# Kernel tuning notes

Measured on AMD Instinct MI355X. Metric: run time of the kernel, lower is better.

Reference implementation:

```python
import jax, jax.numpy as jnp
import numpy as np

B, N, D_MODEL, ATT_DIM, H = 2, 2048, 1024, 1024, 8
HEAD_DIM = ATT_DIM // H


def setup_inputs() -> dict:
    key = jax.random.key(0)
    ks = jax.random.split(key, 10)
    s_in = 1.0 / np.sqrt(D_MODEL)
    s_att = 1.0 / np.sqrt(ATT_DIM)
    x = jax.random.normal(ks[0], (B, N, D_MODEL), dtype=jnp.float32)
    mask = jax.random.randint(ks[1], (B, 1, N, N), 0, 2) == 1
    Wq = jax.random.uniform(ks[2], (D_MODEL, ATT_DIM), jnp.float32, -s_in, s_in)
    bq = jnp.zeros((ATT_DIM,), jnp.float32)
    Wk = jax.random.uniform(ks[3], (D_MODEL, ATT_DIM), jnp.float32, -s_in, s_in)
    bk = jnp.zeros((ATT_DIM,), jnp.float32)
    Wv = jax.random.uniform(ks[4], (D_MODEL, ATT_DIM), jnp.float32, -s_in, s_in)
    bv = jnp.zeros((ATT_DIM,), jnp.float32)
    Wo = jax.random.uniform(ks[5], (ATT_DIM, D_MODEL), jnp.float32, -s_att, s_att)
    bo = jnp.zeros((D_MODEL,), jnp.float32)
    return {"x": x, "mask": mask, "Wq": Wq, "bq": bq, "Wk": Wk, "bk": bk,
            "Wv": Wv, "bv": bv, "Wo": Wo, "bo": bo}


def reference(x, mask, Wq, bq, Wk, bk, Wv, bv, Wo, bo):
    # x: [B, N, d_model]; dropout is identity (eval mode) for a deterministic baseline.
    b, n, d_model = x.shape
    scale = d_model ** (-0.5)  # NOTE: original scales by d_model, not head_dim

    def split_heads(t):  # [B, N, att] -> [B, H, N, head]
        return t.reshape(b, n, H, HEAD_DIM).transpose(0, 2, 1, 3)

    q = split_heads(x @ Wq + bq)
    k = split_heads(x @ Wk + bk)
    v = split_heads(x @ Wv + bv)
    score = jnp.einsum('bhqd,bhkd->bhqk', q, k) * scale
    score = jnp.where(mask, -jnp.inf, score)
    w = jax.nn.softmax(score, axis=-1)
    out = jnp.einsum('bhqk,bhkd->bhqd', w, v)            # [B, H, N, head]
    out = out.transpose(0, 2, 1, 3).reshape(b, n, ATT_DIM)
    return out @ Wo + bo
```

## Files before the change

kernel.cpp:

```cpp
#include <hip/hip_runtime.h>
#include <stdint.h>

typedef __bf16 bf16_t;
typedef bf16_t bf16x8 __attribute__((ext_vector_type(8)));
typedef float f32x4 __attribute__((ext_vector_type(4)));
typedef unsigned long long u64;

#define B_ 2
#define N_ 2048
#define DM 1024
#define H_ 8
#define HD 128

#define GLDS16(g, l) __builtin_amdgcn_global_load_lds(                      \
    (const __attribute__((address_space(1))) void*)(g),                     \
    (__attribute__((address_space(3))) void*)(l), 16, 0, 0)

__global__ void cvt_kernel(const float* __restrict__ in, bf16_t* __restrict__ out, int n8)
{
    int i = blockIdx.x * blockDim.x + threadIdx.x;
    if (i >= n8) return;
    const float4 a = *(const float4*)(in + (size_t)i * 8);
    const float4 b = *(const float4*)(in + (size_t)i * 8 + 4);
    bf16x8 o;
    o[0] = (bf16_t)a.x; o[1] = (bf16_t)a.y; o[2] = (bf16_t)a.z; o[3] = (bf16_t)a.w;
    o[4] = (bf16_t)b.x; o[5] = (bf16_t)b.y; o[6] = (bf16_t)b.z; o[7] = (bf16_t)b.w;
    *(bf16x8*)(out + (size_t)i * 8) = o;
}

__global__ void transpose_cvt(const float* __restrict__ W, bf16_t* __restrict__ Wt)
{
    __shared__ float t[32][33];
    const int tx = threadIdx.x & 31;
    const int ty = threadIdx.x >> 5;
    const int bx = blockIdx.x * 32;
    const int by = blockIdx.y * 32;
#pragma unroll
    for (int i = 0; i < 32; i += 8)
        t[ty + i][tx] = W[(size_t)(by + ty + i) * 1024 + bx + tx];
    __syncthreads();
#pragma unroll
    for (int i = 0; i < 32; i += 8)
        Wt[(size_t)(bx + ty + i) * 1024 + by + tx] = (bf16_t)t[tx][ty + i];
}

__global__ void mask_pack(const int* __restrict__ mask, u64* __restrict__ mb, int nwords)
{
    const int t = blockIdx.x * blockDim.x + threadIdx.x;
    const int w = t >> 6;
    if (w >= nwords) return;
    const int v = mask[(size_t)w * 64 + (t & 63)];
    const u64 bits = __ballot(v != 0);
    if ((t & 63) == 0) mb[w] = bits;
}

template<int MODE>
__global__ __launch_bounds__(256)
void gemm_bt(const bf16_t* __restrict__ A, const bf16_t* __restrict__ Bt,
             const float* __restrict__ b0, const float* __restrict__ b1,
             const float* __restrict__ b2,
             void* __restrict__ Cout, bf16_t* __restrict__ VtOut,
             const int M, const int N, const int K, const int ldc)
{
    __shared__ bf16_t sA[2][128 * 32];
    __shared__ bf16_t sB[2][128 * 32];

    const int tid  = threadIdx.x;
    const int wv   = tid >> 6;
    const int lane = tid & 63;
    const int fr   = lane & 15;
    const int fk   = (lane >> 4) * 8;

    const int row0 = blockIdx.x * 128;
    const int col0 = blockIdx.y * 128;
    const int wr   = (wv >> 1) * 64;
    const int wc   = (wv & 1) * 64;

    const int srow = wv * 32 + (lane >> 2);
    const int scol = (lane & 3) * 8;

    const bf16_t* gA0 = A  + (size_t)(row0 + srow) * K + scol;
    const bf16_t* gA1 = gA0 + (size_t)16 * K;
    const bf16_t* gB0 = Bt + (size_t)(col0 + srow) * K + scol;
    const bf16_t* gB1 = gB0 + (size_t)16 * K;

    const int ldst0 = wv * 1024;
    const int ldst1 = wv * 1024 + 512;

    f32x4 acc[4][4] = {};
    const int NT = K >> 5;

    GLDS16(gA0, &sA[0][ldst0]);
    GLDS16(gA1, &sA[0][ldst1]);
    GLDS16(gB0, &sB[0][ldst0]);
    GLDS16(gB1, &sB[0][ldst1]);
    __syncthreads();

    for (int kt = 0; kt < NT; ++kt) {
        const int cur = kt & 1;
        if (kt + 1 < NT) {
            const size_t ko = (size_t)(kt + 1) * 32;
            GLDS16(gA0 + ko, &sA[cur ^ 1][ldst0]);
            GLDS16(gA1 + ko, &sA[cur ^ 1][ldst1]);
            GLDS16(gB0 + ko, &sB[cur ^ 1][ldst0]);
            GLDS16(gB1 + ko, &sB[cur ^ 1][ldst1]);
        }
        bf16x8 af[4], bfr[4];
#pragma unroll
        for (int i = 0; i < 4; ++i)
            af[i] = *(const bf16x8*)&sA[cur][(wr + i * 16 + fr) * 32 + fk];
#pragma unroll
        for (int i = 0; i < 4; ++i)
            bfr[i] = *(const bf16x8*)&sB[cur][(wc + i * 16 + fr) * 32 + fk];
#pragma unroll
        for (int i = 0; i < 4; ++i)
#pragma unroll
            for (int j = 0; j < 4; ++j)
                acc[i][j] = __builtin_amdgcn_mfma_f32_16x16x32_bf16(af[i], bfr[j], acc[i][j], 0, 0, 0);
        __syncthreads();
    }

#pragma unroll
    for (int i = 0; i < 4; ++i) {
#pragma unroll
        for (int j = 0; j < 4; ++j) {
            const int c = col0 + wc + j * 16 + fr;
            const int seg = c >> 10;
            const float bb = (seg == 0) ? b0[c] : (seg == 1 ? b1[c - 1024] : b2[c - 2048]);
#pragma unroll
            for (int r = 0; r < 4; ++r) {
                const int row = row0 + wr + i * 16 + (lane >> 4) * 4 + r;
                const float v = acc[i][j][r] + bb;
                if constexpr (MODE == 1) {
                    ((float*)Cout)[(size_t)row * ldc + c] = v;
                } else if constexpr (MODE == 0) {
                    ((bf16_t*)Cout)[(size_t)row * ldc + c] = (bf16_t)v;
                } else {
                    if (c < 2048) {
                        ((bf16_t*)Cout)[(size_t)row * ldc + c] = (bf16_t)v;
                    } else {
                        const int ch = c - 2048;
                        const int bb_ = row >> 11;
                        const int nn  = row & 2047;
                        VtOut[((size_t)(bb_ * H_ + (ch >> 7)) * HD + (ch & 127)) * N_ + nn] = (bf16_t)v;
                    }
                }
            }
        }
    }
}

__global__ __launch_bounds__(256)
void flash_attn(const bf16_t* __restrict__ QK, const bf16_t* __restrict__ Vt,
                const u64* __restrict__ mbits, bf16_t* __restrict__ AO)
{
    __shared__ bf16_t sK[64 * 128];
    __shared__ bf16_t sVt[128 * 64];
    __shared__ bf16_t sP[4][16 * 64];

    const int tid  = threadIdx.x;
    const int wv   = tid >> 6;
    const int lane = tid & 63;
    const int fr   = lane & 15;
    const int g4   = lane >> 4;
    const int fk   = g4 * 8;

    const int bh = blockIdx.x & 15;
    const int q0 = (blockIdx.x >> 4) * 64;
    const int b  = bh >> 3;
    const int h  = bh & 7;

    const int qrow = q0 + wv * 16 + fr;
    const size_t qoff = ((size_t)(b * N_ + qrow)) * 2048 + h * HD;
    bf16x8 qf[4];
#pragma unroll
    for (int j = 0; j < 4; ++j) {
        bf16x8 t = *(const bf16x8*)&QK[qoff + j * 32 + fk];
#pragma unroll
        for (int e = 0; e < 8; ++e) qf[j][e] = (bf16_t)((float)t[e] * 0.03125f);
    }

    const bf16_t* kg[4]; bf16_t* kd[4];
#pragma unroll
    for (int n = 0; n < 4; ++n) {
        const int row = wv * 16 + n * 4 + g4;
        kg[n] = QK + ((size_t)(b * N_ + row)) * 2048 + 1024 + h * HD
                   + ((fr * 8) ^ ((row & 15) << 3));
        kd[n] = sK + (wv * 16 + n * 4) * 128;
    }
    const bf16_t* vg[4]; bf16_t* vd[4];
    {
        const int l8 = lane >> 3;
        const int c8 = (lane & 7) * 8;
#pragma unroll
        for (int n = 0; n < 4; ++n) {
            const int d = wv * 32 + n * 8 + l8;
            vg[n] = Vt + ((size_t)((b * H_ + h) * HD + d)) * N_ + (c8 ^ (l8 << 3));
            vd[n] = sVt + (wv * 32 + n * 8) * 64;
        }
    }
    const size_t mrow = (size_t)(b * N_ + q0 + wv * 16 + g4 * 4) * 32;

    f32x4 acc_o[8] = {};
    float mr[4], ls[4];
#pragma unroll
    for (int r = 0; r < 4; ++r) { mr[r] = -1e30f; ls[r] = 0.0f; }

    const int ksw = fr << 3;
    const int vsw = (fr & 7) << 3;
    const int psw = ((fr & 7) << 3) ^ ((fr & 8) << 1);

    for (int kc = 0; kc < N_ / 64; ++kc) {
        __syncthreads();
#pragma unroll
        for (int n = 0; n < 4; ++n) {
            GLDS16(kg[n] + (size_t)kc * 64 * 2048, kd[n]);
            GLDS16(vg[n] + kc * 64, vd[n]);
        }
        u64 mb[4];
#pragma unroll
        for (int r = 0; r < 4; ++r) mb[r] = mbits[mrow + (size_t)r * 32 + kc];
        __syncthreads();

        f32x4 accs[4] = {};
#pragma unroll
        for (int kf = 0; kf < 4; ++kf) {
            const int krow = kf * 16 + fr;
#pragma unroll
            for (int j = 0; j < 4; ++j) {
                bf16x8 kb = *(const bf16x8*)&sK[krow * 128 + ((j * 32 + fk) ^ ksw)];
                accs[kf] = __builtin_amdgcn_mfma_f32_16x16x32_bf16(qf[j], kb, accs[kf], 0, 0, 0);
            }
        }

        float sv[4][4];
#pragma unroll
        for (int kf = 0; kf < 4; ++kf)
#pragma unroll
            for (int r = 0; r < 4; ++r)
                sv[kf][r] = ((mb[r] >> (kf * 16 + fr)) & 1ull) ? -__builtin_inff()
                                                               : accs[kf][r];

        float al[4];
#pragma unroll
        for (int r = 0; r < 4; ++r) {
            float v = fmaxf(fmaxf(sv[0][r], sv[1][r]), fmaxf(sv[2][r], sv[3][r]));
#pragma unroll
            for (int mm = 1; mm <= 8; mm <<= 1) v = fmaxf(v, __shfl_xor(v, mm, 16));
            const float mnew = fmaxf(mr[r], v);
            al[r] = __expf(mr[r] - mnew);
            mr[r] = mnew;
        }
        float ps[4] = {0.f, 0.f, 0.f, 0.f};
#pragma unroll
        for (int kf = 0; kf < 4; ++kf) {
#pragma unroll
            for (int r = 0; r < 4; ++r) {
                const float p = __expf(sv[kf][r] - mr[r]);
                ps[r] += p;
                const int prow = g4 * 4 + r;
                const int s = ((prow & 7) << 3) ^ ((prow & 8) << 1);
                sP[wv][prow * 64 + ((kf * 16 + fr) ^ s)] = (bf16_t)p;
            }
        }
#pragma unroll
        for (int r = 0; r < 4; ++r) {
            float v = ps[r];
#pragma unroll
            for (int mm = 1; mm <= 8; mm <<= 1) v += __shfl_xor(v, mm, 16);
            ls[r] = ls[r] * al[r] + v;
        }
#pragma unroll
        for (int df = 0; df < 8; ++df)
#pragma unroll
            for (int r = 0; r < 4; ++r)
                acc_o[df][r] *= al[r];

#pragma unroll
        for (int ks = 0; ks < 2; ++ks) {
            bf16x8 pf = *(const bf16x8*)&sP[wv][fr * 64 + ((ks * 32 + fk) ^ psw)];
#pragma unroll
            for (int df = 0; df < 8; ++df) {
                const int vrow = df * 16 + fr;
                bf16x8 vb = *(const bf16x8*)&sVt[vrow * 64 + ((ks * 32 + fk) ^ vsw)];
                acc_o[df] = __builtin_amdgcn_mfma_f32_16x16x32_bf16(pf, vb, acc_o[df], 0, 0, 0);
            }
        }
    }

#pragma unroll
    for (int df = 0; df < 8; ++df) {
#pragma unroll
        for (int r = 0; r < 4; ++r) {
            const int row = q0 + wv * 16 + g4 * 4 + r;
            AO[((size_t)(b * N_ + row)) * DM + h * HD + df * 16 + fr] =
                (bf16_t)(acc_o[df][r] / ls[r]);
        }
    }
}

extern "C" void kernel_launch(void* const* d_in, const int* in_sizes, int n_in,
                              void* d_out, int out_size, void* d_ws, size_t ws_size,
                              hipStream_t stream)
{
    const float* x  = (const float*)d_in[0];
    const int* mask = (const int*)d_in[1];
    const float* Wq = (const float*)d_in[2];
    const float* bq = (const float*)d_in[3];
    const float* Wk = (const float*)d_in[4];
    const float* bk = (const float*)d_in[5];
    const float* Wv = (const float*)d_in[6];
    const float* bv = (const float*)d_in[7];
    const float* Wo = (const float*)d_in[8];
    const float* bo = (const float*)d_in[9];
    float* out = (float*)d_out;

    const size_t MT = (size_t)B_ * N_;
    bf16_t* xb    = (bf16_t*)d_ws;
    bf16_t* Wqkvt = xb + MT * DM;
    bf16_t* Wot   = Wqkvt + (size_t)3072 * DM;
    bf16_t* QKb   = Wot + (size_t)DM * DM;
    bf16_t* Vtb   = QKb + MT * 2048;
    bf16_t* AOb   = Vtb + (size_t)B_ * H_ * HD * N_;
    u64*    mbits = (u64*)(AOb + MT * DM);

    cvt_kernel<<<2048, 256, 0, stream>>>(x, xb, (int)(MT * DM / 8));

    dim3 tg(32, 32);
    transpose_cvt<<<tg, 256, 0, stream>>>(Wq, Wqkvt);
    transpose_cvt<<<tg, 256, 0, stream>>>(Wk, Wqkvt + (size_t)DM * DM);
    transpose_cvt<<<tg, 256, 0, stream>>>(Wv, Wqkvt + (size_t)2 * DM * DM);
    transpose_cvt<<<tg, 256, 0, stream>>>(Wo, Wot);

    const int nwords = B_ * N_ * (N_ / 64);
    mask_pack<<<nwords / 4, 256, 0, stream>>>(mask, mbits, nwords);

    gemm_bt<2><<<dim3(MT / 128, 3072 / 128), 256, 0, stream>>>(
        xb, Wqkvt, bq, bk, bv, QKb, Vtb, (int)MT, 3072, DM, 2048);

    flash_attn<<<512, 256, 0, stream>>>(QKb, Vtb, mbits, AOb);

    gemm_bt<1><<<dim3(MT / 128, DM / 128), 256, 0, stream>>>(
        AOb, Wot, bo, bo, bo, out, nullptr, (int)MT, DM, DM, DM);
}
```

Before: 287.9 us.

## Split attention KV range in two, drop online max, swizzle GEMM block order

Flash attention now splits the key/value sequence into two halves across twice as many workgroups. Each half writes a partial normalized output and its row sum, and a new combine kernel merges the two halves by weighting them with those sums. The online max tracking and accumulator rescaling are removed: exp is taken of raw scaled scores, and row sums are computed with an MFMA against a ones vector. This cuts VALU and shuffle work, but it assumes the scores stay small enough not to overflow. Both GEMMs switch to a 1D grid whose block index is swizzled in groups of eight, and the attention kernel gets a waves-per-EU launch bound; the buffer for the partial outputs reuses the workspace that held the converted x.

```diff
diff --git a/kernel.cpp b/kernel.cpp
--- a/kernel.cpp
+++ b/kernel.cpp
@@ -3,6 +3,7 @@
 
 typedef __bf16 bf16_t;
 typedef bf16_t bf16x8 __attribute__((ext_vector_type(8)));
+typedef bf16_t bf16x4 __attribute__((ext_vector_type(4)));
 typedef float f32x4 __attribute__((ext_vector_type(4)));
 typedef unsigned long long u64;
 
@@ -60,7 +61,7 @@
              const float* __restrict__ b0, const float* __restrict__ b1,
              const float* __restrict__ b2,
              void* __restrict__ Cout, bf16_t* __restrict__ VtOut,
-             const int M, const int N, const int K, const int ldc)
+             const int M, const int N, const int K, const int ldc, const int gy)
 {
     __shared__ bf16_t sA[2][128 * 32];
     __shared__ bf16_t sB[2][128 * 32];
@@ -71,8 +72,13 @@
     const int fr   = lane & 15;
     const int fk   = (lane >> 4) * 8;
 
-    const int row0 = blockIdx.x * 128;
-    const int col0 = blockIdx.y * 128;
+    const int nwg = gridDim.x;
+    const int swz = ((int)blockIdx.x & 7) * (nwg >> 3) + ((int)blockIdx.x >> 3);
+    const int by  = swz % gy;
+    const int bx  = swz / gy;
+
+    const int row0 = bx * 128;
+    const int col0 = by * 128;
     const int wr   = (wv >> 1) * 64;
     const int wc   = (wv & 1) * 64;
 
@@ -150,9 +156,10 @@
     }
 }
 
-__global__ __launch_bounds__(256)
+__global__ __launch_bounds__(256, 4)
 void flash_attn(const bf16_t* __restrict__ QK, const bf16_t* __restrict__ Vt,
-                const u64* __restrict__ mbits, bf16_t* __restrict__ AO)
+                const u64* __restrict__ mbits, bf16_t* __restrict__ Os,
+                float* __restrict__ Ls)
 {
     __shared__ bf16_t sK[64 * 128];
     __shared__ bf16_t sVt[128 * 64];
@@ -165,10 +172,13 @@
     const int g4   = lane >> 4;
     const int fk   = g4 * 8;
 
-    const int bh = blockIdx.x & 15;
-    const int q0 = (blockIdx.x >> 4) * 64;
+    const int work = ((int)blockIdx.x & 7) * 128 + ((int)blockIdx.x >> 3);
+    const int s  = work >> 9;
+    const int bh = (work >> 5) & 15;
+    const int q0 = (work & 31) * 64;
     const int b  = bh >> 3;
     const int h  = bh & 7;
+    const int kvbase = s * 1024;
 
     const int qrow = q0 + wv * 16 + fr;
     const size_t qoff = ((size_t)(b * N_ + qrow)) * 2048 + h * HD;
@@ -184,7 +194,7 @@
 #pragma unroll
     for (int n = 0; n < 4; ++n) {
         const int row = wv * 16 + n * 4 + g4;
-        kg[n] = QK + ((size_t)(b * N_ + row)) * 2048 + 1024 + h * HD
+        kg[n] = QK + ((size_t)(b * N_ + kvbase + row)) * 2048 + 1024 + h * HD
                    + ((fr * 8) ^ ((row & 15) << 3));
         kd[n] = sK + (wv * 16 + n * 4) * 128;
     }
@@ -195,22 +205,25 @@
 #pragma unroll
         for (int n = 0; n < 4; ++n) {
             const int d = wv * 32 + n * 8 + l8;
-            vg[n] = Vt + ((size_t)((b * H_ + h) * HD + d)) * N_ + (c8 ^ (l8 << 3));
+            vg[n] = Vt + ((size_t)((b * H_ + h) * HD + d)) * N_ + kvbase + (c8 ^ (l8 << 3));
             vd[n] = sVt + (wv * 32 + n * 8) * 64;
         }
     }
-    const size_t mrow = (size_t)(b * N_ + q0 + wv * 16 + g4 * 4) * 32;
+    const size_t mrow = (size_t)(b * N_ + q0 + wv * 16 + g4 * 4) * 32 + s * 16;
 
     f32x4 acc_o[8] = {};
-    float mr[4], ls[4];
-#pragma unroll
-    for (int r = 0; r < 4; ++r) { mr[r] = -1e30f; ls[r] = 0.0f; }
+    f32x4 acc_l = {};
+    bf16x8 ones_f = {};
+    if (fr == 0) {
+#pragma unroll
+        for (int e = 0; e < 8; ++e) ones_f[e] = (bf16_t)1.0f;
+    }
 
     const int ksw = fr << 3;
     const int vsw = (fr & 7) << 3;
     const int psw = ((fr & 7) << 3) ^ ((fr & 8) << 1);
 
-    for (int kc = 0; kc < N_ / 64; ++kc) {
+    for (int kc = 0; kc < 16; ++kc) {
         __syncthreads();
 #pragma unroll
         for (int n = 0; n < 4; ++n) {
@@ -233,52 +246,23 @@
             }
         }
 
-        float sv[4][4];
-#pragma unroll
-        for (int kf = 0; kf < 4; ++kf)
-#pragma unroll
-            for (int r = 0; r < 4; ++r)
-                sv[kf][r] = ((mb[r] >> (kf * 16 + fr)) & 1ull) ? -__builtin_inff()
-                                                               : accs[kf][r];
-
-        float al[4];
-#pragma unroll
-        for (int r = 0; r < 4; ++r) {
-            float v = fmaxf(fmaxf(sv[0][r], sv[1][r]), fmaxf(sv[2][r], sv[3][r]));
-#pragma unroll
-            for (int mm = 1; mm <= 8; mm <<= 1) v = fmaxf(v, __shfl_xor(v, mm, 16));
-            const float mnew = fmaxf(mr[r], v);
-            al[r] = __expf(mr[r] - mnew);
-            mr[r] = mnew;
-        }
-        float ps[4] = {0.f, 0.f, 0.f, 0.f};
 #pragma unroll
         for (int kf = 0; kf < 4; ++kf) {
 #pragma unroll
             for (int r = 0; r < 4; ++r) {
-                const float p = __expf(sv[kf][r] - mr[r]);
-                ps[r] += p;
+                const float svv = ((mb[r] >> (kf * 16 + fr)) & 1ull) ? -__builtin_inff()
+                                                                     : accs[kf][r];
+                const float p = __expf(svv);
                 const int prow = g4 * 4 + r;
-                const int s = ((prow & 7) << 3) ^ ((prow & 8) << 1);
-                sP[wv][prow * 64 + ((kf * 16 + fr) ^ s)] = (bf16_t)p;
+                const int ss = ((prow & 7) << 3) ^ ((prow & 8) << 1);
+                sP[wv][prow * 64 + ((kf * 16 + fr) ^ ss)] = (bf16_t)p;
             }
         }
-#pragma unroll
-        for (int r = 0; r < 4; ++r) {
-            float v = ps[r];
-#pragma unroll
-            for (int mm = 1; mm <= 8; mm <<= 1) v += __shfl_xor(v, mm, 16);
-            ls[r] = ls[r] * al[r] + v;
-        }
-#pragma unroll
-        for (int df = 0; df < 8; ++df)
-#pragma unroll
-            for (int r = 0; r < 4; ++r)
-                acc_o[df][r] *= al[r];
 
 #pragma unroll
         for (int ks = 0; ks < 2; ++ks) {
             bf16x8 pf = *(const bf16x8*)&sP[wv][fr * 64 + ((ks * 32 + fk) ^ psw)];
+            acc_l = __builtin_amdgcn_mfma_f32_16x16x32_bf16(pf, ones_f, acc_l, 0, 0, 0);
 #pragma unroll
             for (int df = 0; df < 8; ++df) {
                 const int vrow = df * 16 + fr;
@@ -288,15 +272,50 @@
         }
     }
 
+    float lv[4], inv[4];
+#pragma unroll
+    for (int r = 0; r < 4; ++r) {
+        lv[r]  = __shfl(acc_l[r], lane & 48, 64);
+        inv[r] = 1.0f / lv[r];
+    }
+
 #pragma unroll
     for (int df = 0; df < 8; ++df) {
 #pragma unroll
         for (int r = 0; r < 4; ++r) {
             const int row = q0 + wv * 16 + g4 * 4 + r;
-            AO[((size_t)(b * N_ + row)) * DM + h * HD + df * 16 + fr] =
-                (bf16_t)(acc_o[df][r] / ls[r]);
-        }
-    }
+            Os[((size_t)(s * 4096 + b * N_ + row)) * 1024 + h * 128 + df * 16 + fr] =
+                (bf16_t)(acc_o[df][r] * inv[r]);
+        }
+    }
+    if (fr == 0) {
+#pragma unroll
+        for (int r = 0; r < 4; ++r) {
+            const int row = q0 + wv * 16 + g4 * 4 + r;
+            Ls[((size_t)((s * 2 + b) * 8 + h)) * 2048 + row] = lv[r];
+        }
+    }
+}
+
+__global__ void combine(const bf16_t* __restrict__ Os, const float* __restrict__ Ls,
+                        bf16_t* __restrict__ AO)
+{
+    const int i = blockIdx.x;
+    const int c = threadIdx.x * 4;
+    const int b = i >> 11;
+    const int n = i & 2047;
+    const int h = c >> 7;
+    const float l0 = Ls[((size_t)(b * 8 + h)) * 2048 + n];
+    const float l1 = Ls[((size_t)(16 + b * 8 + h)) * 2048 + n];
+    const float w  = 1.0f / (l0 + l1);
+    const float w0 = l0 * w, w1 = l1 * w;
+    bf16x4 a = *(const bf16x4*)&Os[(size_t)i * 1024 + c];
+    bf16x4 d = *(const bf16x4*)&Os[(size_t)4096 * 1024 + (size_t)i * 1024 + c];
+    bf16x4 o;
+#pragma unroll
+    for (int e = 0; e < 4; ++e)
+        o[e] = (bf16_t)((float)a[e] * w0 + (float)d[e] * w1);
+    *(bf16x4*)&AO[(size_t)i * 1024 + c] = o;
 }
 
 extern "C" void kernel_launch(void* const* d_in, const int* in_sizes, int n_in,
@@ -316,13 +335,17 @@
     float* out = (float*)d_out;
 
     const size_t MT = (size_t)B_ * N_;
-    bf16_t* xb    = (bf16_t*)d_ws;
-    bf16_t* Wqkvt = xb + MT * DM;
-    bf16_t* Wot   = Wqkvt + (size_t)3072 * DM;
-    bf16_t* QKb   = Wot + (size_t)DM * DM;
+    const size_t M1 = 1024 * 1024;
+    bf16_t* wsb   = (bf16_t*)d_ws;
+    bf16_t* Os    = wsb;
+    bf16_t* xb    = wsb;
+    bf16_t* Wqkvt = wsb + 4 * M1;
+    bf16_t* Wot   = wsb + 8 * M1;
+    bf16_t* QKb   = wsb + 9 * M1;
     bf16_t* Vtb   = QKb + MT * 2048;
     bf16_t* AOb   = Vtb + (size_t)B_ * H_ * HD * N_;
     u64*    mbits = (u64*)(AOb + MT * DM);
+    float*  Ls    = (float*)(mbits + (size_t)B_ * N_ * 32);
 
     cvt_kernel<<<2048, 256, 0, stream>>>(x, xb, (int)(MT * DM / 8));
 
@@ -335,11 +358,13 @@
     const int nwords = B_ * N_ * (N_ / 64);
     mask_pack<<<nwords / 4, 256, 0, stream>>>(mask, mbits, nwords);
 
-    gemm_bt<2><<<dim3(MT / 128, 3072 / 128), 256, 0, stream>>>(
-        xb, Wqkvt, bq, bk, bv, QKb, Vtb, (int)MT, 3072, DM, 2048);
-
-    flash_attn<<<512, 256, 0, stream>>>(QKb, Vtb, mbits, AOb);
-
-    gemm_bt<1><<<dim3(MT / 128, DM / 128), 256, 0, stream>>>(
-        AOb, Wot, bo, bo, bo, out, nullptr, (int)MT, DM, DM, DM);
-}
+    gemm_bt<2><<<768, 256, 0, stream>>>(
+        xb, Wqkvt, bq, bk, bv, QKb, Vtb, (int)MT, 3072, DM, 2048, 24);
+
+    flash_attn<<<1024, 256, 0, stream>>>(QKb, Vtb, mbits, Os, Ls);
+
+    combine<<<4096, 256, 0, stream>>>(Os, Ls, AOb);
+
+    gemm_bt<1><<<256, 256, 0, stream>>>(
+        AOb, Wot, bo, bo, bo, out, nullptr, (int)MT, DM, DM, DM, 8);
+}
```

Measured after the change: 274.8 us. 1.05x faster.
